# Optimization experiments

Hardware: AMD Instinct MI355X
Metric: run time of the kernel (lower is better)

The kernel has to match this reference:

```python
import jax, jax.numpy as jnp
import numpy as np

B, C, H, W = 32, 512, 24, 8
C8 = C // 8  # PAM query/key channels


def setup_inputs() -> dict:
    key = jax.random.key(0)
    k0, k1, k2, k3, k4 = jax.random.split(key, 5)
    x = jax.random.normal(k0, (B, C, H, W), dtype=jnp.float32)
    Wq = jax.random.normal(k1, (C8, C), dtype=jnp.float32) * 0.02
    bq = jnp.zeros((C8,), dtype=jnp.float32)
    Wk = jax.random.normal(k2, (C8, C), dtype=jnp.float32) * 0.02
    bk = jnp.zeros((C8,), dtype=jnp.float32)
    return {"x": x, "Wq": Wq, "bq": bq, "Wk": Wk, "bk": bk}


def reference(x, Wq, bq, Wk, bk):
    b, c, h, w = x.shape
    hw = h * w
    xf = x.reshape(b, c, hw)  # [B, C, hw]

    # QAConv: einsum('gchw,pcyx->gpyxhw') with kernel == x, then view(B,-1,hw,hw).
    # With m=(h,w) of features and n=(y,x) of kernel this is 'gcm,pcn->gpnm'.
    score = jnp.einsum('gcm,pcn->gpnm', xf, xf)  # [B, B, hw, hw]
    kernel_max = score.max(axis=3)               # max over feature positions -> [B, B, hw]

    # PAM: 1x1 conv projections then bmm(q^T, k).
    q = jnp.einsum('qc,bcm->bqm', Wq, xf) + bq[None, :, None]  # [B, C8, hw]
    k = jnp.einsum('qc,bcm->bqm', Wk, xf) + bk[None, :, None]  # [B, C8, hw]
    energy = jnp.einsum('bqm,bqn->bmn', q, k)                  # [B, hw, hw]
    pos_max = energy.max(axis=2)[None]                         # [1, B, hw]

    return jnp.concatenate([kernel_max, pos_max], axis=0)  # [B+1, B, hw]
```

## Files before the change

### kernel.cpp

```cpp
#include <hip/hip_runtime.h>

typedef __bf16 bf16x8 __attribute__((ext_vector_type(8)));
typedef float f32x4 __attribute__((ext_vector_type(4)));
typedef unsigned short u16x8 __attribute__((ext_vector_type(8)));
typedef unsigned short u16x4 __attribute__((ext_vector_type(4)));

#define B_ 32
#define CC 512
#define HW 192
#define C8_ 64
#define NTRI 528
#define FBUF_B 24576

__device__ inline unsigned short f2bf(float f) {
    unsigned u = __float_as_uint(f);
    unsigned r = (u + 0x7FFFu + ((u >> 16) & 1u)) >> 16;
    return (unsigned short)r;
}

__device__ inline void gload16(const void* g, void* l) {
    __builtin_amdgcn_global_load_lds(
        (const __attribute__((address_space(1))) unsigned*)g,
        (__attribute__((address_space(3))) unsigned*)l,
        16, 0, 0);
}

__global__ void prep(const float* __restrict__ x,
                     const float* __restrict__ Wq, const float* __restrict__ Wk,
                     unsigned short* __restrict__ xt,
                     unsigned short* __restrict__ wqb, unsigned short* __restrict__ wkb) {
    __shared__ unsigned short tile[64 * 64];
    int t = threadIdx.x;
    if (blockIdx.x >= 96) {
        int id = (blockIdx.x - 96) * 8 + blockIdx.y;
        const float* src = (id < 32) ? Wq : Wk;
        unsigned short* dst = (id < 32) ? wqb : wkb;
        int base = (id & 31) * 1024 + t * 4;
        f32x4 a = *(const f32x4*)(src + base);
        u16x4 o;
        #pragma unroll
        for (int e = 0; e < 4; ++e) o[e] = f2bf(a[e]);
        *(u16x4*)(dst + base) = o;
        return;
    }
    int b = blockIdx.x / 3, mt = blockIdx.x % 3;
    int m0 = mt * 64, c0 = blockIdx.y * 64;
    const float* xb = x + (size_t)b * CC * HW + (size_t)c0 * HW + m0;

    int mq = t & 15, cl0 = t >> 4;
    int sw = (mq & 7) << 3;
    #pragma unroll
    for (int rd = 0; rd < 4; ++rd) {
        int cl = rd * 16 + cl0;
        f32x4 v = *(const f32x4*)(xb + cl * HW + mq * 4);
        #pragma unroll
        for (int e = 0; e < 4; ++e)
            tile[(mq * 4 + e) * 64 + (cl ^ sw)] = f2bf(v[e]);
    }
    __syncthreads();
    unsigned short* xo = xt + ((size_t)b * HW + m0) * CC + c0;
    int kc = t & 7, mr0 = t >> 3;
    #pragma unroll
    for (int rd = 0; rd < 2; ++rd) {
        int mr = rd * 32 + mr0;
        u16x8 v = *(const u16x8*)&tile[mr * 64 + ((kc << 3) ^ (((mr >> 2) & 7) << 3))];
        *(u16x8*)(xo + (size_t)mr * CC + kc * 8) = v;
    }
}

__global__ __launch_bounds__(256) void pam_qk(
        const unsigned short* __restrict__ xt,
        const unsigned short* __restrict__ wqb, const unsigned short* __restrict__ wkb,
        const float* __restrict__ bq, const float* __restrict__ bk,
        unsigned short* __restrict__ qo, unsigned short* __restrict__ ko) {
    int b = blockIdx.x, m0 = blockIdx.y * 48;
    int tid = threadIdx.x, w = tid >> 6, lane = tid & 63;
    int l15 = lane & 15, lq = lane >> 4;
    int qc = w * 16 + l15;

    f32x4 accq[3], acck[3];
    #pragma unroll
    for (int i = 0; i < 3; ++i) {
        accq[i] = (f32x4){0.f, 0.f, 0.f, 0.f};
        acck[i] = (f32x4){0.f, 0.f, 0.f, 0.f};
    }

    const unsigned short* xb = xt + ((size_t)b * HW + m0) * CC;
    const unsigned short* wqp = wqb + (size_t)qc * CC;
    const unsigned short* wkp = wkb + (size_t)qc * CC;

    for (int kt = 0; kt < 16; ++kt) {
        int ko8 = kt * 32 + lq * 8;
        bf16x8 wqf = *(const bf16x8*)(wqp + ko8);
        bf16x8 wkf = *(const bf16x8*)(wkp + ko8);
        bf16x8 af[3];
        #pragma unroll
        for (int i = 0; i < 3; ++i)
            af[i] = *(const bf16x8*)(xb + (i * 16 + l15) * CC + ko8);
        #pragma unroll
        for (int i = 0; i < 3; ++i) {
            accq[i] = __builtin_amdgcn_mfma_f32_16x16x32_bf16(af[i], wqf, accq[i], 0, 0, 0);
            acck[i] = __builtin_amdgcn_mfma_f32_16x16x32_bf16(af[i], wkf, acck[i], 0, 0, 0);
        }
    }

    float bqv = bq[qc], bkv = bk[qc];
    #pragma unroll
    for (int i = 0; i < 3; ++i) {
        #pragma unroll
        for (int r = 0; r < 4; ++r) {
            int m = m0 + i * 16 + lq * 4 + r;
            qo[((size_t)b * HW + m) * C8_ + qc] = f2bf(accq[i][r] + bqv);
            ko[((size_t)b * HW + m) * C8_ + qc] = f2bf(acck[i][r] + bkv);
        }
    }
}

__global__ __launch_bounds__(256, 2) void gram5(const unsigned short* __restrict__ xt,
                                                float* __restrict__ out) {
    __shared__ __attribute__((aligned(16))) char smem[2 * FBUF_B];

    int tid = threadIdx.x;
    int bid = (blockIdx.x & 7) * 66 + (blockIdx.x >> 3);
    int idx = bid, g = 0;
    while (idx >= B_ - g) { idx -= B_ - g; ++g; }
    int p = g + idx;

    const unsigned short* xg = xt + (size_t)g * HW * CC;
    const unsigned short* xp = xt + (size_t)p * HW * CC;

    int w = tid >> 6, lane = tid & 63;
    int wr = w >> 1, wc = w & 1;
    int l15 = lane & 15, lq = lane >> 4;

    int sc = ((tid & 3) ^ ((tid >> 3) & 3)) << 3;
    const unsigned short* baseA = xg + (size_t)(tid >> 2) * CC + sc;
    const unsigned short* baseB = xp + (size_t)(tid >> 2) * CC + sc;
    unsigned ldsA = (unsigned)tid * 16;

    unsigned aoff[6], boff[6];
    #pragma unroll
    for (int i = 0; i < 6; ++i) {
        int row = wr * 96 + i * 16 + l15;
        aoff[i] = (unsigned)row * 64 + ((unsigned)(lq ^ ((row >> 1) & 3)) << 4);
    }
    #pragma unroll
    for (int j = 0; j < 6; ++j) {
        int n = wc * 96 + j * 16 + l15;
        boff[j] = 12288u + (unsigned)n * 64 + ((unsigned)(lq ^ ((n >> 1) & 3)) << 4);
    }

    f32x4 acc[6][6];
    #pragma unroll
    for (int i = 0; i < 6; ++i)
        #pragma unroll
        for (int j = 0; j < 6; ++j)
            acc[i][j] = (f32x4){0.f, 0.f, 0.f, 0.f};

    #define STG5(buf, kt)                                                      \
        {                                                                      \
            char* base = smem + (buf) * FBUF_B;                                \
            int k0 = (kt) * 32;                                                \
            _Pragma("unroll")                                                  \
            for (int ci = 0; ci < 3; ++ci) {                                   \
                gload16(baseA + k0 + ci * 64 * CC, base + ldsA + ci * 4096);   \
                gload16(baseB + k0 + ci * 64 * CC,                             \
                        base + 12288 + ldsA + ci * 4096);                      \
            }                                                                  \
        }

    #define CMP5(buf)                                                          \
        {                                                                      \
            const char* Bb = smem + (buf) * FBUF_B;                            \
            bf16x8 bfr[6];                                                     \
            _Pragma("unroll")                                                  \
            for (int j = 0; j < 6; ++j)                                        \
                bfr[j] = *(const bf16x8*)(Bb + boff[j]);                       \
            _Pragma("unroll")                                                  \
            for (int i = 0; i < 6; ++i) {                                      \
                bf16x8 a = *(const bf16x8*)(Bb + aoff[i]);                     \
                _Pragma("unroll")                                              \
                for (int j = 0; j < 6; ++j)                                    \
                    acc[i][j] = __builtin_amdgcn_mfma_f32_16x16x32_bf16(       \
                        a, bfr[j], acc[i][j], 0, 0, 0);                        \
            }                                                                  \
        }

    STG5(0, 0);
    __syncthreads();
    for (int kt = 0; kt < 16; ++kt) {
        int cur = kt & 1;
        if (kt < 15) STG5(cur ^ 1, kt + 1);
        CMP5(cur);
        __syncthreads();
    }

    float* colbuf = (float*)smem;
    float* rowbuf = (float*)(smem + 1536);

    #pragma unroll
    for (int i = 0; i < 6; ++i) {
        float rm[4];
        #pragma unroll
        for (int r = 0; r < 4; ++r) rm[r] = -1e30f;
        #pragma unroll
        for (int j = 0; j < 6; ++j)
            #pragma unroll
            for (int r = 0; r < 4; ++r)
                rm[r] = fmaxf(rm[r], acc[i][j][r]);
        #pragma unroll
        for (int msk = 1; msk <= 8; msk <<= 1)
            #pragma unroll
            for (int r = 0; r < 4; ++r)
                rm[r] = fmaxf(rm[r], __shfl_xor(rm[r], msk));
        if (l15 == 0) {
            #pragma unroll
            for (int r = 0; r < 4; ++r)
                rowbuf[wc * HW + wr * 96 + i * 16 + lq * 4 + r] = rm[r];
        }
    }
    #pragma unroll
    for (int j = 0; j < 6; ++j) {
        float cm = -1e30f;
        #pragma unroll
        for (int i = 0; i < 6; ++i)
            #pragma unroll
            for (int r = 0; r < 4; ++r)
                cm = fmaxf(cm, acc[i][j][r]);
        cm = fmaxf(cm, __shfl_xor(cm, 16));
        cm = fmaxf(cm, __shfl_xor(cm, 32));
        if (lane < 16) colbuf[wr * HW + wc * 96 + j * 16 + l15] = cm;
    }
    __syncthreads();
    if (tid < HW) {
        float cmax = fmaxf(colbuf[tid], colbuf[HW + tid]);
        out[((size_t)g * B_ + p) * HW + tid] = cmax;
        float rmax = fmaxf(rowbuf[tid], rowbuf[HW + tid]);
        out[((size_t)p * B_ + g) * HW + tid] = rmax;
    }
}

__global__ __launch_bounds__(256) void pam_energy(
        const unsigned short* __restrict__ qo,
        const unsigned short* __restrict__ ko,
        float* __restrict__ out) {
    int b = blockIdx.x, m0 = blockIdx.y * 48;
    int tid = threadIdx.x, w = tid >> 6, lane = tid & 63;
    int l15 = lane & 15, lq = lane >> 4;
    int n0 = w * 48;

    f32x4 acc[3][3];
    #pragma unroll
    for (int i = 0; i < 3; ++i)
        #pragma unroll
        for (int j = 0; j < 3; ++j)
            acc[i][j] = (f32x4){0.f, 0.f, 0.f, 0.f};

    const unsigned short* qb = qo + ((size_t)b * HW + m0) * C8_;
    const unsigned short* kb = ko + ((size_t)b * HW + n0) * C8_;

    #pragma unroll
    for (int kt = 0; kt < 2; ++kt) {
        int ko8 = kt * 32 + lq * 8;
        bf16x8 af[3], bfr[3];
        #pragma unroll
        for (int i = 0; i < 3; ++i)
            af[i] = *(const bf16x8*)(qb + (i * 16 + l15) * C8_ + ko8);
        #pragma unroll
        for (int j = 0; j < 3; ++j)
            bfr[j] = *(const bf16x8*)(kb + (j * 16 + l15) * C8_ + ko8);
        #pragma unroll
        for (int i = 0; i < 3; ++i)
            #pragma unroll
            for (int j = 0; j < 3; ++j)
                acc[i][j] = __builtin_amdgcn_mfma_f32_16x16x32_bf16(af[i], bfr[j], acc[i][j], 0, 0, 0);
    }

    __shared__ float red[4][48];
    #pragma unroll
    for (int i = 0; i < 3; ++i) {
        float rm[4];
        #pragma unroll
        for (int r = 0; r < 4; ++r) rm[r] = -1e30f;
        #pragma unroll
        for (int j = 0; j < 3; ++j)
            #pragma unroll
            for (int r = 0; r < 4; ++r)
                rm[r] = fmaxf(rm[r], acc[i][j][r]);
        #pragma unroll
        for (int msk = 1; msk <= 8; msk <<= 1)
            #pragma unroll
            for (int r = 0; r < 4; ++r)
                rm[r] = fmaxf(rm[r], __shfl_xor(rm[r], msk));
        if (l15 == 0) {
            #pragma unroll
            for (int r = 0; r < 4; ++r)
                red[w][i * 16 + lq * 4 + r] = rm[r];
        }
    }
    __syncthreads();
    if (tid < 48) {
        float v = fmaxf(fmaxf(red[0][tid], red[1][tid]),
                        fmaxf(red[2][tid], red[3][tid]));
        out[((size_t)B_ * B_ + b) * HW + m0 + tid] = v;
    }
}

extern "C" void kernel_launch(void* const* d_in, const int* in_sizes, int n_in,
                              void* d_out, int out_size, void* d_ws, size_t ws_size,
                              hipStream_t stream) {
    (void)in_sizes; (void)n_in; (void)out_size; (void)ws_size;
    const float* x  = (const float*)d_in[0];
    const float* Wq = (const float*)d_in[1];
    const float* bq = (const float*)d_in[2];
    const float* Wk = (const float*)d_in[3];
    const float* bk = (const float*)d_in[4];
    float* out = (float*)d_out;

    char* ws = (char*)d_ws;
    unsigned short* xt  = (unsigned short*)ws;
    unsigned short* wqb = (unsigned short*)(ws + 6291456);
    unsigned short* wkb = (unsigned short*)(ws + 6291456 + 65536);
    unsigned short* qbuf = (unsigned short*)(ws + 6291456 + 131072);
    unsigned short* kbuf = (unsigned short*)(ws + 6291456 + 131072 + 786432);

    prep<<<dim3(104, 8), dim3(256), 0, stream>>>(x, Wq, Wk, xt, wqb, wkb);
    pam_qk<<<dim3(32, 4), dim3(256), 0, stream>>>(xt, wqb, wkb, bq, bk, qbuf, kbuf);
    gram5<<<dim3(NTRI), dim3(256), 0, stream>>>(xt, out);
    pam_energy<<<dim3(32, 4), dim3(256), 0, stream>>>(qbuf, kbuf, out);
}
```

Before: 58.42 us.

## Fuse Q/K projection into gram kernel and widen gram blocks to 512 threads

```diff
diff --git a/kernel.cpp b/kernel.cpp
--- a/kernel.cpp
+++ b/kernel.cpp
@@ -10,7 +10,8 @@
 #define HW 192
 #define C8_ 64
 #define NTRI 528
-#define FBUF_B 24576
+#define NBLK 656
+#define FB 24576
 
 __device__ inline unsigned short f2bf(float f) {
     unsigned u = __float_as_uint(f);
@@ -68,175 +69,170 @@
     }
 }
 
-__global__ __launch_bounds__(256) void pam_qk(
+__global__ __launch_bounds__(512, 4) void gram_qk(
         const unsigned short* __restrict__ xt,
         const unsigned short* __restrict__ wqb, const unsigned short* __restrict__ wkb,
         const float* __restrict__ bq, const float* __restrict__ bk,
-        unsigned short* __restrict__ qo, unsigned short* __restrict__ ko) {
-    int b = blockIdx.x, m0 = blockIdx.y * 48;
-    int tid = threadIdx.x, w = tid >> 6, lane = tid & 63;
+        unsigned short* __restrict__ qo, unsigned short* __restrict__ ko,
+        float* __restrict__ out) {
+    __shared__ __attribute__((aligned(16))) char smem[2 * FB];
+
+    int tid = threadIdx.x;
+    int w = tid >> 6, lane = tid & 63;
     int l15 = lane & 15, lq = lane >> 4;
-    int qc = w * 16 + l15;
-
-    f32x4 accq[3], acck[3];
-    #pragma unroll
-    for (int i = 0; i < 3; ++i) {
-        accq[i] = (f32x4){0.f, 0.f, 0.f, 0.f};
-        acck[i] = (f32x4){0.f, 0.f, 0.f, 0.f};
-    }
-
-    const unsigned short* xb = xt + ((size_t)b * HW + m0) * CC;
-    const unsigned short* wqp = wqb + (size_t)qc * CC;
-    const unsigned short* wkp = wkb + (size_t)qc * CC;
-
-    for (int kt = 0; kt < 16; ++kt) {
-        int ko8 = kt * 32 + lq * 8;
-        bf16x8 wqf = *(const bf16x8*)(wqp + ko8);
-        bf16x8 wkf = *(const bf16x8*)(wkp + ko8);
-        bf16x8 af[3];
+
+    if (blockIdx.x < NTRI) {
+        int bid = (blockIdx.x & 7) * 66 + (blockIdx.x >> 3);
+        int idx = bid, g = 0;
+        while (idx >= B_ - g) { idx -= B_ - g; ++g; }
+        int p = g + idx;
+
+        const unsigned short* xg = xt + (size_t)g * HW * CC;
+        const unsigned short* xp = xt + (size_t)p * HW * CC;
+
+        int wr = w >> 1, wc = w & 1;
+
+        const unsigned short* sp[3];
+        unsigned lo[3];
+        #pragma unroll
+        for (int ci = 0; ci < 3; ++ci) {
+            int q = tid + 512 * ci;
+            lo[ci] = (unsigned)q * 16;
+            int q2 = (q < 768) ? q : q - 768;
+            int r = q2 >> 2, s = q2 & 3;
+            sp[ci] = ((q < 768) ? xg : xp) + r * CC + ((s ^ ((r >> 1) & 3)) << 3);
+        }
+
+        unsigned aoff[3], boff[6];
+        #pragma unroll
+        for (int i = 0; i < 3; ++i) {
+            int row = wr * 48 + i * 16 + l15;
+            aoff[i] = (unsigned)row * 64 + ((unsigned)(lq ^ ((row >> 1) & 3)) << 4);
+        }
+        #pragma unroll
+        for (int j = 0; j < 6; ++j) {
+            int n = wc * 96 + j * 16 + l15;
+            boff[j] = 12288u + (unsigned)n * 64 + ((unsigned)(lq ^ ((n >> 1) & 3)) << 4);
+        }
+
+        f32x4 acc[3][6];
         #pragma unroll
         for (int i = 0; i < 3; ++i)
-            af[i] = *(const bf16x8*)(xb + (i * 16 + l15) * CC + ko8);
-        #pragma unroll
-        for (int i = 0; i < 3; ++i) {
-            accq[i] = __builtin_amdgcn_mfma_f32_16x16x32_bf16(af[i], wqf, accq[i], 0, 0, 0);
-            acck[i] = __builtin_amdgcn_mfma_f32_16x16x32_bf16(af[i], wkf, acck[i], 0, 0, 0);
-        }
-    }
-
-    float bqv = bq[qc], bkv = bk[qc];
-    #pragma unroll
-    for (int i = 0; i < 3; ++i) {
-        #pragma unroll
-        for (int r = 0; r < 4; ++r) {
-            int m = m0 + i * 16 + lq * 4 + r;
-            qo[((size_t)b * HW + m) * C8_ + qc] = f2bf(accq[i][r] + bqv);
-            ko[((size_t)b * HW + m) * C8_ + qc] = f2bf(acck[i][r] + bkv);
-        }
-    }
-}
-
-__global__ __launch_bounds__(256, 2) void gram5(const unsigned short* __restrict__ xt,
-                                                float* __restrict__ out) {
-    __shared__ __attribute__((aligned(16))) char smem[2 * FBUF_B];
-
-    int tid = threadIdx.x;
-    int bid = (blockIdx.x & 7) * 66 + (blockIdx.x >> 3);
-    int idx = bid, g = 0;
-    while (idx >= B_ - g) { idx -= B_ - g; ++g; }
-    int p = g + idx;
-
-    const unsigned short* xg = xt + (size_t)g * HW * CC;
-    const unsigned short* xp = xt + (size_t)p * HW * CC;
-
-    int w = tid >> 6, lane = tid & 63;
-    int wr = w >> 1, wc = w & 1;
-    int l15 = lane & 15, lq = lane >> 4;
-
-    int sc = ((tid & 3) ^ ((tid >> 3) & 3)) << 3;
-    const unsigned short* baseA = xg + (size_t)(tid >> 2) * CC + sc;
-    const unsigned short* baseB = xp + (size_t)(tid >> 2) * CC + sc;
-    unsigned ldsA = (unsigned)tid * 16;
-
-    unsigned aoff[6], boff[6];
-    #pragma unroll
-    for (int i = 0; i < 6; ++i) {
-        int row = wr * 96 + i * 16 + l15;
-        aoff[i] = (unsigned)row * 64 + ((unsigned)(lq ^ ((row >> 1) & 3)) << 4);
-    }
-    #pragma unroll
-    for (int j = 0; j < 6; ++j) {
-        int n = wc * 96 + j * 16 + l15;
-        boff[j] = 12288u + (unsigned)n * 64 + ((unsigned)(lq ^ ((n >> 1) & 3)) << 4);
-    }
-
-    f32x4 acc[6][6];
-    #pragma unroll
-    for (int i = 0; i < 6; ++i)
-        #pragma unroll
-        for (int j = 0; j < 6; ++j)
-            acc[i][j] = (f32x4){0.f, 0.f, 0.f, 0.f};
-
-    #define STG5(buf, kt)                                                      \
-        {                                                                      \
-            char* base = smem + (buf) * FBUF_B;                                \
-            int k0 = (kt) * 32;                                                \
-            _Pragma("unroll")                                                  \
-            for (int ci = 0; ci < 3; ++ci) {                                   \
-                gload16(baseA + k0 + ci * 64 * CC, base + ldsA + ci * 4096);   \
-                gload16(baseB + k0 + ci * 64 * CC,                             \
-                        base + 12288 + ldsA + ci * 4096);                      \
-            }                                                                  \
-        }
-
-    #define CMP5(buf)                                                          \
-        {                                                                      \
-            const char* Bb = smem + (buf) * FBUF_B;                            \
-            bf16x8 bfr[6];                                                     \
-            _Pragma("unroll")                                                  \
-            for (int j = 0; j < 6; ++j)                                        \
-                bfr[j] = *(const bf16x8*)(Bb + boff[j]);                       \
-            _Pragma("unroll")                                                  \
-            for (int i = 0; i < 6; ++i) {                                      \
-                bf16x8 a = *(const bf16x8*)(Bb + aoff[i]);                     \
+            #pragma unroll
+            for (int j = 0; j < 6; ++j)
+                acc[i][j] = (f32x4){0.f, 0.f, 0.f, 0.f};
+
+        #define STG(buf, kt)                                                   \
+            {                                                                  \
+                char* base = smem + (buf) * FB;                                \
+                int k0 = (kt) * 32;                                            \
+                gload16(sp[0] + k0, base + lo[0]);                             \
+                gload16(sp[1] + k0, base + lo[1]);                             \
+                gload16(sp[2] + k0, base + lo[2]);                             \
+            }
+
+        #define CMP(buf)                                                       \
+            {                                                                  \
+                const char* Bb = smem + (buf) * FB;                            \
+                bf16x8 af[3], bfr[6];                                          \
+                _Pragma("unroll")                                              \
+                for (int i = 0; i < 3; ++i)                                    \
+                    af[i] = *(const bf16x8*)(Bb + aoff[i]);                    \
                 _Pragma("unroll")                                              \
                 for (int j = 0; j < 6; ++j)                                    \
-                    acc[i][j] = __builtin_amdgcn_mfma_f32_16x16x32_bf16(       \
-                        a, bfr[j], acc[i][j], 0, 0, 0);                        \
-            }                                                                  \
-        }
-
-    STG5(0, 0);
-    __syncthreads();
-    for (int kt = 0; kt < 16; ++kt) {
-        int cur = kt & 1;
-        if (kt < 15) STG5(cur ^ 1, kt + 1);
-        CMP5(cur);
+                    bfr[j] = *(const bf16x8*)(Bb + boff[j]);                   \
+                _Pragma("unroll")                                              \
+                for (int i = 0; i < 3; ++i)                                    \
+                    _Pragma("unroll")                                          \
+                    for (int j = 0; j < 6; ++j)                                \
+                        acc[i][j] = __builtin_amdgcn_mfma_f32_16x16x32_bf16(   \
+                            af[i], bfr[j], acc[i][j], 0, 0, 0);                \
+            }
+
+        STG(0, 0);
         __syncthreads();
-    }
-
-    float* colbuf = (float*)smem;
-    float* rowbuf = (float*)(smem + 1536);
-
-    #pragma unroll
-    for (int i = 0; i < 6; ++i) {
-        float rm[4];
-        #pragma unroll
-        for (int r = 0; r < 4; ++r) rm[r] = -1e30f;
-        #pragma unroll
-        for (int j = 0; j < 6; ++j)
-            #pragma unroll
-            for (int r = 0; r < 4; ++r)
-                rm[r] = fmaxf(rm[r], acc[i][j][r]);
-        #pragma unroll
-        for (int msk = 1; msk <= 8; msk <<= 1)
-            #pragma unroll
-            for (int r = 0; r < 4; ++r)
-                rm[r] = fmaxf(rm[r], __shfl_xor(rm[r], msk));
-        if (l15 == 0) {
-            #pragma unroll
-            for (int r = 0; r < 4; ++r)
-                rowbuf[wc * HW + wr * 96 + i * 16 + lq * 4 + r] = rm[r];
-        }
-    }
-    #pragma unroll
-    for (int j = 0; j < 6; ++j) {
-        float cm = -1e30f;
-        #pragma unroll
-        for (int i = 0; i < 6; ++i)
-            #pragma unroll
-            for (int r = 0; r < 4; ++r)
-                cm = fmaxf(cm, acc[i][j][r]);
-        cm = fmaxf(cm, __shfl_xor(cm, 16));
-        cm = fmaxf(cm, __shfl_xor(cm, 32));
-        if (lane < 16) colbuf[wr * HW + wc * 96 + j * 16 + l15] = cm;
-    }
-    __syncthreads();
-    if (tid < HW) {
-        float cmax = fmaxf(colbuf[tid], colbuf[HW + tid]);
-        out[((size_t)g * B_ + p) * HW + tid] = cmax;
-        float rmax = fmaxf(rowbuf[tid], rowbuf[HW + tid]);
-        out[((size_t)p * B_ + g) * HW + tid] = rmax;
+        for (int kt = 0; kt < 16; ++kt) {
+            int cur = kt & 1;
+            if (kt < 15) STG(cur ^ 1, kt + 1);
+            CMP(cur);
+            __syncthreads();
+        }
+
+        float* rowbuf = (float*)smem;
+        float* colbuf = (float*)(smem + 1536);
+
+        #pragma unroll
+        for (int i = 0; i < 3; ++i) {
+            float rm[4];
+            #pragma unroll
+            for (int r = 0; r < 4; ++r) rm[r] = -1e30f;
+            #pragma unroll
+            for (int j = 0; j < 6; ++j)
+                #pragma unroll
+                for (int r = 0; r < 4; ++r)
+                    rm[r] = fmaxf(rm[r], acc[i][j][r]);
+            #pragma unroll
+            for (int msk = 1; msk <= 8; msk <<= 1)
+                #pragma unroll
+                for (int r = 0; r < 4; ++r)
+                    rm[r] = fmaxf(rm[r], __shfl_xor(rm[r], msk));
+            if (l15 == 0) {
+                #pragma unroll
+                for (int r = 0; r < 4; ++r)
+                    rowbuf[wc * HW + wr * 48 + i * 16 + lq * 4 + r] = rm[r];
+            }
+        }
+        #pragma unroll
+        for (int j = 0; j < 6; ++j) {
+            float cm = -1e30f;
+            #pragma unroll
+            for (int i = 0; i < 3; ++i)
+                #pragma unroll
+                for (int r = 0; r < 4; ++r)
+                    cm = fmaxf(cm, acc[i][j][r]);
+            cm = fmaxf(cm, __shfl_xor(cm, 16));
+            cm = fmaxf(cm, __shfl_xor(cm, 32));
+            if (lane < 16) colbuf[wr * HW + wc * 96 + j * 16 + l15] = cm;
+        }
+        __syncthreads();
+        if (tid < HW) {
+            float rmax = fmaxf(rowbuf[tid], rowbuf[HW + tid]);
+            out[((size_t)p * B_ + g) * HW + tid] = rmax;
+            float cmax = fmaxf(fmaxf(colbuf[tid], colbuf[HW + tid]),
+                               fmaxf(colbuf[2 * HW + tid], colbuf[3 * HW + tid]));
+            out[((size_t)g * B_ + p) * HW + tid] = cmax;
+        }
+    } else {
+        int pb = blockIdx.x - NTRI;
+        int b = pb >> 2, m0 = (pb & 3) * 48;
+        int w4 = w & 3;
+        int qc = w4 * 16 + l15;
+        bool isq = (w < 4);
+        const unsigned short* wp = (isq ? wqb : wkb) + (size_t)qc * CC;
+        float bias = isq ? bq[qc] : bk[qc];
+        unsigned short* dst = isq ? qo : ko;
+        const unsigned short* xb = xt + ((size_t)b * HW + m0) * CC;
+
+        f32x4 a3[3];
+        #pragma unroll
+        for (int i = 0; i < 3; ++i) a3[i] = (f32x4){0.f, 0.f, 0.f, 0.f};
+        for (int kt = 0; kt < 16; ++kt) {
+            int ko8 = kt * 32 + lq * 8;
+            bf16x8 wf = *(const bf16x8*)(wp + ko8);
+            #pragma unroll
+            for (int i = 0; i < 3; ++i) {
+                bf16x8 af = *(const bf16x8*)(xb + (i * 16 + l15) * CC + ko8);
+                a3[i] = __builtin_amdgcn_mfma_f32_16x16x32_bf16(af, wf, a3[i], 0, 0, 0);
+            }
+        }
+        #pragma unroll
+        for (int i = 0; i < 3; ++i) {
+            #pragma unroll
+            for (int r = 0; r < 4; ++r) {
+                int m = m0 + i * 16 + lq * 4 + r;
+                dst[((size_t)b * HW + m) * C8_ + qc] = f2bf(a3[i][r] + bias);
+            }
+        }
     }
 }
 
@@ -325,7 +321,7 @@
     unsigned short* kbuf = (unsigned short*)(ws + 6291456 + 131072 + 786432);
 
     prep<<<dim3(104, 8), dim3(256), 0, stream>>>(x, Wq, Wk, xt, wqb, wkb);
-    pam_qk<<<dim3(32, 4), dim3(256), 0, stream>>>(xt, wqb, wkb, bq, bk, qbuf, kbuf);
-    gram5<<<dim3(NTRI), dim3(256), 0, stream>>>(xt, out);
+    gram_qk<<<dim3(NBLK), dim3(512), 0, stream>>>(
+        xt, wqb, wkb, bq, bk, qbuf, kbuf, out);
     pam_energy<<<dim3(32, 4), dim3(256), 0, stream>>>(qbuf, kbuf, out);
 }
```

After: 63.51 us. +8.7%, slower.
